# Kernel tuning notes

Hardware: AMD Instinct MI355X
Metric: run time of the kernel (lower is better)

The kernel has to match this reference:

```python
import jax, jax.numpy as jnp
import numpy as np

N_NODES = 50000
N_EDGES = 800000
IN_DIM, HID, OUT_DIM = 128, 64, 64


def setup_inputs() -> dict:
    key = jax.random.key(0)
    ks = jax.random.split(key, 12)
    inp = {
        "x": jax.random.normal(ks[0], (N_NODES, IN_DIM), dtype=jnp.float32),
        "edge_index": jax.random.randint(ks[1], (2, N_EDGES), 0, N_NODES, dtype=jnp.int32),
    }
    dims = [(IN_DIM, HID), (HID, HID), (HID, HID), (HID, HID), (HID, OUT_DIM)]
    for i, (di, do) in enumerate(dims, start=1):
        scale = (2.0 / (di + do)) ** 0.5  # glorot-like
        inp[f"W{i}"] = jax.random.normal(ks[1 + i], (di, do), dtype=jnp.float32) * scale
        inp[f"b{i}"] = jnp.zeros((do,), dtype=jnp.float32)
    return inp


def _edge_norm(edge_index, n_nodes):
    # GCNConv(improved=True): add self-loops with weight 2.0, symmetric norm.
    src, dst = edge_index[0], edge_index[1]
    loop = jnp.arange(n_nodes, dtype=edge_index.dtype)
    src_f = jnp.concatenate([src, loop])
    dst_f = jnp.concatenate([dst, loop])
    w = jnp.concatenate([
        jnp.ones((src.shape[0],), jnp.float32),
        jnp.full((n_nodes,), 2.0, jnp.float32),
    ])
    deg = jax.ops.segment_sum(w, dst_f, num_segments=n_nodes)
    dinv = jnp.where(deg > 0, jax.lax.rsqrt(deg), 0.0)
    norm = dinv[src_f] * w * dinv[dst_f]  # [E+N]
    return src_f, dst_f, norm


def reference(x, edge_index, W1, b1, W2, b2, W3, b3, W4, b4, W5, b5):
    n = x.shape[0]
    src_f, dst_f, norm = _edge_norm(edge_index, n)

    def conv(h, W, b):
        h = h @ W                                  # [N, d_out]
        msg = h[src_f] * norm[:, None]             # gather + edge normalize
        return jax.ops.segment_sum(msg, dst_f, num_segments=n) + b

    h = jax.nn.relu(conv(x, W1, b1))
    h = jax.nn.relu(conv(h, W2, b2))
    h = jax.nn.relu(conv(h, W3, b3))
    h = jax.nn.relu(conv(h, W4, b4))
    return conv(h, W5, b5)
```

## Files before the change

### kernel.cpp

```cpp
#include <hip/hip_runtime.h>
#include <hip/hip_fp16.h>

#define NN 50000
#define NE 800000

__device__ __forceinline__ float bf2f(unsigned short u) {
    union { unsigned int i; float f; } v; v.i = ((unsigned int)u) << 16; return v.f;
}
__device__ __forceinline__ unsigned short f2bf(float f) {
    union { float f; unsigned int i; } v; v.f = f;
    unsigned int r = v.i + 0x7fffu + ((v.i >> 16) & 1u);
    return (unsigned short)(r >> 16);
}
__device__ __forceinline__ float rdlane_f(float x, int l) {
    return __uint_as_float(__builtin_amdgcn_readlane(__float_as_uint(x), l));
}

__global__ void k_zero(float4* __restrict__ p, int n16) {
    int i = blockIdx.x * 256 + threadIdx.x;
    if (i < n16) p[i] = make_float4(0.f, 0.f, 0.f, 0.f);
}


__global__ void k_count(const int* __restrict__ dst, int* __restrict__ cnt, int E) {
    int e = blockIdx.x * 256 + threadIdx.x;
    if (e < E) atomicAdd(&cnt[dst[e]], 1);
}

__global__ void k_scanA(const int* __restrict__ cnt, int* __restrict__ row_ptr,
                        int* __restrict__ bsum, float* __restrict__ dinv, int N) {
    __shared__ int buf[256];
    int i = blockIdx.x * 256 + threadIdx.x;
    int v = (i < N) ? cnt[i] : 0;
    if (i < N) dinv[i] = rsqrtf(2.0f + (float)v);
    buf[threadIdx.x] = v;
    __syncthreads();
    for (int off = 1; off < 256; off <<= 1) {
        int t = (threadIdx.x >= off) ? buf[threadIdx.x - off] : 0;
        __syncthreads();
        buf[threadIdx.x] += t;
        __syncthreads();
    }
    if (i < N) row_ptr[i] = buf[threadIdx.x] - v;
    if (threadIdx.x == 255) bsum[blockIdx.x] = buf[255];
}

__global__ void k_scanB(int* __restrict__ bsum, int nb) {
    __shared__ int buf[256];
    int v = (threadIdx.x < nb) ? bsum[threadIdx.x] : 0;
    buf[threadIdx.x] = v;
    __syncthreads();
    for (int off = 1; off < 256; off <<= 1) {
        int t = (threadIdx.x >= off) ? buf[threadIdx.x - off] : 0;
        __syncthreads();
        buf[threadIdx.x] += t;
        __syncthreads();
    }
    if (threadIdx.x < nb) bsum[threadIdx.x] = buf[threadIdx.x] - v;
}

__global__ void k_scanC(int* __restrict__ row_ptr, const int* __restrict__ bsum,
                        int N, int E) {
    int i = blockIdx.x * 256 + threadIdx.x;
    if (i < N) row_ptr[i] += bsum[blockIdx.x];
    if (i == 0) row_ptr[N] = E;
}

__global__ void k_fill(const int* __restrict__ src, const int* __restrict__ dst,
                       const float* __restrict__ dinv, const int* __restrict__ row_ptr,
                       int* __restrict__ cursor, unsigned* __restrict__ csr, int E) {
    int e = blockIdx.x * 256 + threadIdx.x;
    if (e >= E) return;
    int s = src[e], d = dst[e];
    int pos = row_ptr[d] + atomicAdd(&cursor[d], 1);
    float nm = dinv[s] * dinv[d];
    csr[pos] = (unsigned)s | ((unsigned)__half_as_ushort(__float2half(nm)) << 16);
}


__global__ __launch_bounds__(256, 4) void k_gemm128(const float* __restrict__ X,
                                                    const float* __restrict__ W,
                                                    unsigned short* __restrict__ H, int N) {
    const int K = 128;
    __shared__ float Ws[K * 64];
    for (int i = threadIdx.x; i < K * 16; i += 256)
        ((float4*)Ws)[i] = ((const float4*)W)[i];
    __syncthreads();

    const int g  = threadIdx.x >> 3;
    const int c0 = (threadIdx.x & 7) * 8;
    const int r0 = blockIdx.x * 64 + g * 2;
    const int r1 = r0 + 1;
    const bool v0 = r0 < N, v1 = r1 < N;

    float a00=0,a01=0,a02=0,a03=0,a04=0,a05=0,a06=0,a07=0;
    float a10=0,a11=0,a12=0,a13=0,a14=0,a15=0,a16=0,a17=0;

    const float* x0 = X + (size_t)r0 * K;
    const float* x1 = X + (size_t)r1 * K;

#pragma unroll 1
    for (int k0 = 0; k0 < K; k0 += 4) {
        float4 xa = v0 ? *(const float4*)(x0 + k0) : make_float4(0, 0, 0, 0);
        float4 xb = v1 ? *(const float4*)(x1 + k0) : make_float4(0, 0, 0, 0);
#pragma unroll
        for (int kk = 0; kk < 4; ++kk) {
            const float xs0 = (kk == 0) ? xa.x : (kk == 1) ? xa.y : (kk == 2) ? xa.z : xa.w;
            const float xs1 = (kk == 0) ? xb.x : (kk == 1) ? xb.y : (kk == 2) ? xb.z : xb.w;
            const float* wr = &Ws[(k0 + kk) * 64 + c0];
            const float4 w0 = *(const float4*)(wr);
            const float4 w1 = *(const float4*)(wr + 4);
            a00 = fmaf(xs0, w0.x, a00); a01 = fmaf(xs0, w0.y, a01);
            a02 = fmaf(xs0, w0.z, a02); a03 = fmaf(xs0, w0.w, a03);
            a04 = fmaf(xs0, w1.x, a04); a05 = fmaf(xs0, w1.y, a05);
            a06 = fmaf(xs0, w1.z, a06); a07 = fmaf(xs0, w1.w, a07);
            a10 = fmaf(xs1, w0.x, a10); a11 = fmaf(xs1, w0.y, a11);
            a12 = fmaf(xs1, w0.z, a12); a13 = fmaf(xs1, w0.w, a13);
            a14 = fmaf(xs1, w1.x, a14); a15 = fmaf(xs1, w1.y, a15);
            a16 = fmaf(xs1, w1.z, a16); a17 = fmaf(xs1, w1.w, a17);
        }
    }

    if (v0) {
        uint4 p;
        p.x = (unsigned)f2bf(a00) | ((unsigned)f2bf(a01) << 16);
        p.y = (unsigned)f2bf(a02) | ((unsigned)f2bf(a03) << 16);
        p.z = (unsigned)f2bf(a04) | ((unsigned)f2bf(a05) << 16);
        p.w = (unsigned)f2bf(a06) | ((unsigned)f2bf(a07) << 16);
        *(uint4*)&H[(size_t)r0 * 64 + c0] = p;
    }
    if (v1) {
        uint4 p;
        p.x = (unsigned)f2bf(a10) | ((unsigned)f2bf(a11) << 16);
        p.y = (unsigned)f2bf(a12) | ((unsigned)f2bf(a13) << 16);
        p.z = (unsigned)f2bf(a14) | ((unsigned)f2bf(a15) << 16);
        p.w = (unsigned)f2bf(a16) | ((unsigned)f2bf(a17) << 16);
        *(uint4*)&H[(size_t)r1 * 64 + c0] = p;
    }
}


__device__ __forceinline__ void unpack(unsigned w, int& ss, float& nn) {
    ss = (int)(w & 0xffffu);
    nn = __half2float(__ushort_as_half((unsigned short)(w >> 16)));
}

template <bool RELU>
__device__ __forceinline__ void agg_row2(const unsigned short* __restrict__ H,
                                         const unsigned* __restrict__ csr,
                                         const float4& b4, float di0, float di1,
                                         int i0, int i1, int s0, int e0, int s1, int e1,
                                         int lane, int g, int c4,
                                         float4& r0, float4& r1) {
    ushort4 hs0 = *(const ushort4*)&H[(size_t)i0 * 64 + c4];
    ushort4 hs1 = *(const ushort4*)&H[(size_t)i1 * 64 + c4];

    int ee0 = s0 + lane, ee1 = s1 + lane;
    unsigned pk0 = (ee0 < e0) ? csr[ee0] : 0u;
    unsigned pk1 = (ee1 < e1) ? csr[ee1] : 0u;

    int m0 = e0 - s0; if (m0 > 64) m0 = 64;
    int m1 = e1 - s1; if (m1 > 64) m1 = 64;
    int nt0 = (m0 + 3) >> 2, nt1 = (m1 + 3) >> 2;
    int ntm = nt0 > nt1 ? nt0 : nt1;

    float4 acc0 = make_float4(0.f, 0.f, 0.f, 0.f);
    float4 acc1 = make_float4(0.f, 0.f, 0.f, 0.f);

#pragma unroll 4
    for (int t = 0; t < ntm; ++t) {
        int sl = t * 4 + g;
        if (t < nt0) {
            unsigned w = __shfl(pk0, sl);
            int ss; float nn; unpack(w, ss, nn);
            ushort4 h = *(const ushort4*)&H[(size_t)ss * 64 + c4];
            acc0.x = fmaf(bf2f(h.x), nn, acc0.x);
            acc0.y = fmaf(bf2f(h.y), nn, acc0.y);
            acc0.z = fmaf(bf2f(h.z), nn, acc0.z);
            acc0.w = fmaf(bf2f(h.w), nn, acc0.w);
        }
        if (t < nt1) {
            unsigned w = __shfl(pk1, sl);
            int ss; float nn; unpack(w, ss, nn);
            ushort4 h = *(const ushort4*)&H[(size_t)ss * 64 + c4];
            acc1.x = fmaf(bf2f(h.x), nn, acc1.x);
            acc1.y = fmaf(bf2f(h.y), nn, acc1.y);
            acc1.z = fmaf(bf2f(h.z), nn, acc1.z);
            acc1.w = fmaf(bf2f(h.w), nn, acc1.w);
        }
    }

    for (int base = s0 + 64; base < e0; base += 64) {
        int e = base + lane;
        unsigned pk = (e < e0) ? csr[e] : 0u;
        int m = e0 - base; if (m > 64) m = 64;
        int nt = (m + 3) >> 2;
        for (int t = 0; t < nt; ++t) {
            unsigned w = __shfl(pk, t * 4 + g);
            int ss; float nn; unpack(w, ss, nn);
            ushort4 h = *(const ushort4*)&H[(size_t)ss * 64 + c4];
            acc0.x = fmaf(bf2f(h.x), nn, acc0.x);
            acc0.y = fmaf(bf2f(h.y), nn, acc0.y);
            acc0.z = fmaf(bf2f(h.z), nn, acc0.z);
            acc0.w = fmaf(bf2f(h.w), nn, acc0.w);
        }
    }
    for (int base = s1 + 64; base < e1; base += 64) {
        int e = base + lane;
        unsigned pk = (e < e1) ? csr[e] : 0u;
        int m = e1 - base; if (m > 64) m = 64;
        int nt = (m + 3) >> 2;
        for (int t = 0; t < nt; ++t) {
            unsigned w = __shfl(pk, t * 4 + g);
            int ss; float nn; unpack(w, ss, nn);
            ushort4 h = *(const ushort4*)&H[(size_t)ss * 64 + c4];
            acc1.x = fmaf(bf2f(h.x), nn, acc1.x);
            acc1.y = fmaf(bf2f(h.y), nn, acc1.y);
            acc1.z = fmaf(bf2f(h.z), nn, acc1.z);
            acc1.w = fmaf(bf2f(h.w), nn, acc1.w);
        }
    }

#pragma unroll
    for (int d = 16; d <= 32; d <<= 1) {
        acc0.x += __shfl_xor(acc0.x, d); acc0.y += __shfl_xor(acc0.y, d);
        acc0.z += __shfl_xor(acc0.z, d); acc0.w += __shfl_xor(acc0.w, d);
        acc1.x += __shfl_xor(acc1.x, d); acc1.y += __shfl_xor(acc1.y, d);
        acc1.z += __shfl_xor(acc1.z, d); acc1.w += __shfl_xor(acc1.w, d);
    }

    float sa = 2.0f * di0 * di0, sb = 2.0f * di1 * di1;
    r0.x = acc0.x + sa * bf2f(hs0.x) + b4.x;
    r0.y = acc0.y + sa * bf2f(hs0.y) + b4.y;
    r0.z = acc0.z + sa * bf2f(hs0.z) + b4.z;
    r0.w = acc0.w + sa * bf2f(hs0.w) + b4.w;
    r1.x = acc1.x + sb * bf2f(hs1.x) + b4.x;
    r1.y = acc1.y + sb * bf2f(hs1.y) + b4.y;
    r1.z = acc1.z + sb * bf2f(hs1.z) + b4.z;
    r1.w = acc1.w + sb * bf2f(hs1.w) + b4.w;
    if (RELU) {
        r0.x = fmaxf(r0.x, 0.f); r0.y = fmaxf(r0.y, 0.f);
        r0.z = fmaxf(r0.z, 0.f); r0.w = fmaxf(r0.w, 0.f);
        r1.x = fmaxf(r1.x, 0.f); r1.y = fmaxf(r1.y, 0.f);
        r1.z = fmaxf(r1.z, 0.f); r1.w = fmaxf(r1.w, 0.f);
    }
}

__global__ __launch_bounds__(256, 8) void k_fused(const unsigned short* __restrict__ H,
                                                  const int* __restrict__ row_ptr,
                                                  const unsigned* __restrict__ csr,
                                                  const float* __restrict__ dinv,
                                                  const float* __restrict__ bias,
                                                  const float* __restrict__ Wn,
                                                  unsigned short* __restrict__ Hout, int N) {
    const int wid  = threadIdx.x >> 6;
    const int lane = threadIdx.x & 63;
    const int i0   = (blockIdx.x * 4 + wid) * 2;
    const int i1   = i0 + 1;
    const int g    = lane >> 4;
    const int c4   = (lane & 15) * 4;

    int idx = i0 + lane;
    int   rp = (lane <= 2) ? row_ptr[idx] : 0;
    float dv = (lane <  2) ? dinv[idx]    : 0.f;

    const float4 b4 = *(const float4*)&bias[c4];
    int s0 = __shfl(rp, 0), sm = __shfl(rp, 1), e1 = __shfl(rp, 2);
    float di0 = __shfl(dv, 0), di1 = __shfl(dv, 1);

    float4 r0, r1;
    agg_row2<true>(H, csr, b4, di0, di1, i0, i1, s0, sm, sm, e1,
                   lane, g, c4, r0, r1);

    float y0 = 0.f, y1 = 0.f;
#pragma unroll
    for (int q = 0; q < 16; ++q) {
        float w0 = Wn[(4 * q + 0) * 64 + lane];
        float w1 = Wn[(4 * q + 1) * 64 + lane];
        float w2 = Wn[(4 * q + 2) * 64 + lane];
        float w3 = Wn[(4 * q + 3) * 64 + lane];
        y0 = fmaf(rdlane_f(r0.x, q), w0, y0);
        y0 = fmaf(rdlane_f(r0.y, q), w1, y0);
        y0 = fmaf(rdlane_f(r0.z, q), w2, y0);
        y0 = fmaf(rdlane_f(r0.w, q), w3, y0);
        y1 = fmaf(rdlane_f(r1.x, q), w0, y1);
        y1 = fmaf(rdlane_f(r1.y, q), w1, y1);
        y1 = fmaf(rdlane_f(r1.z, q), w2, y1);
        y1 = fmaf(rdlane_f(r1.w, q), w3, y1);
    }
    Hout[(size_t)i0 * 64 + lane] = f2bf(y0);
    Hout[(size_t)i1 * 64 + lane] = f2bf(y1);
}

__global__ __launch_bounds__(256, 8) void k_agg_last(const unsigned short* __restrict__ H,
                                                     const int* __restrict__ row_ptr,
                                                     const unsigned* __restrict__ csr,
                                                     const float* __restrict__ dinv,
                                                     const float* __restrict__ bias,
                                                     float* __restrict__ out, int N) {
    const int wid  = threadIdx.x >> 6;
    const int lane = threadIdx.x & 63;
    const int i0   = (blockIdx.x * 4 + wid) * 2;
    const int i1   = i0 + 1;
    const int g    = lane >> 4;
    const int c4   = (lane & 15) * 4;

    const float4 b4 = *(const float4*)&bias[c4];

    int idx = i0 + lane;
    int   rp = (lane <= 2) ? row_ptr[idx] : 0;
    float dv = (lane <  2) ? dinv[idx]    : 0.f;
    int s0 = __shfl(rp, 0), sm = __shfl(rp, 1), e1 = __shfl(rp, 2);
    float di0 = __shfl(dv, 0), di1 = __shfl(dv, 1);

    float4 r0, r1;
    agg_row2<false>(H, csr, b4, di0, di1, i0, i1, s0, sm, sm, e1,
                    lane, g, c4, r0, r1);
    if (g == 0) {
        *(float4*)&out[(size_t)i0 * 64 + c4] = r0;
        *(float4*)&out[(size_t)i1 * 64 + c4] = r1;
    }
}


extern "C" void kernel_launch(void* const* d_in, const int* in_sizes, int n_in,
                              void* d_out, int out_size, void* d_ws, size_t ws_size,
                              hipStream_t stream) {
    (void)in_sizes; (void)n_in; (void)out_size; (void)ws_size;

    const float* x  = (const float*)d_in[0];
    const int*   ei = (const int*)d_in[1];
    const float* Wl[5] = {(const float*)d_in[2], (const float*)d_in[4], (const float*)d_in[6],
                          (const float*)d_in[8], (const float*)d_in[10]};
    const float* bl[5] = {(const float*)d_in[3], (const float*)d_in[5], (const float*)d_in[7],
                          (const float*)d_in[9], (const float*)d_in[11]};
    float* out = (float*)d_out;

    const int* src = ei;
    const int* dst = ei + NE;

    char* ws = (char*)d_ws;
    size_t off = 0;
    auto alloc = [&](size_t bytes) -> void* {
        void* p = ws + off;
        off += (bytes + 255) & ~(size_t)255;
        return p;
    };
    int*      cnt     = (int*)alloc(NN * 4);
    int*      cursor  = (int*)alloc(NN * 4);
    size_t zero_bytes = (size_t)((char*)(cursor + NN) - (char*)cnt);
    int*      row_ptr = (int*)alloc((NN + 1) * 4);
    int*      bsum    = (int*)alloc(256 * 4);
    float*    dinv    = (float*)alloc(NN * 4);
    unsigned* csr     = (unsigned*)alloc((size_t)NE * 4);
    unsigned short* Hb  = (unsigned short*)alloc((size_t)NN * 64 * 2);
    unsigned short* Hb2 = (unsigned short*)alloc((size_t)NN * 64 * 2);

    int n16 = (int)((zero_bytes + 15) / 16);
    k_zero<<<(n16 + 255) / 256, 256, 0, stream>>>((float4*)cnt, n16);

    int ebl = (NE + 255) / 256;
    int nbl = (NN + 255) / 256;
    int gg  = (NN + 63) / 64;
    k_count<<<ebl, 256, 0, stream>>>(dst, cnt, NE);
    k_scanA<<<nbl, 256, 0, stream>>>(cnt, row_ptr, bsum, dinv, NN);
    k_scanB<<<1, 256, 0, stream>>>(bsum, nbl);
    k_scanC<<<nbl, 256, 0, stream>>>(row_ptr, bsum, NN, NE);
    k_fill<<<ebl, 256, 0, stream>>>(src, dst, dinv, row_ptr, cursor, csr, NE);
    k_gemm128<<<gg, 256, 0, stream>>>(x, Wl[0], Hb, NN);

    int ga = NN / 8;

    k_fused<<<ga, 256, 0, stream>>>(Hb,  row_ptr, csr, dinv, bl[0], Wl[1], Hb2, NN);
    k_fused<<<ga, 256, 0, stream>>>(Hb2, row_ptr, csr, dinv, bl[1], Wl[2], Hb,  NN);
    k_fused<<<ga, 256, 0, stream>>>(Hb,  row_ptr, csr, dinv, bl[2], Wl[3], Hb2, NN);
    k_fused<<<ga, 256, 0, stream>>>(Hb2, row_ptr, csr, dinv, bl[3], Wl[4], Hb,  NN);
    k_agg_last<<<ga, 256, 0, stream>>>(Hb, row_ptr, csr, dinv, bl[4], out, NN);
}
```

Measured before the change: 270.0 us.

## Split feature matrix into two column planes and aggregate each half separately

Stores the bf16 hidden features as two planes of 32 columns each, so each aggregation pass gathers a 3.2MB plane that fits better in cache. Each layer is split into two kernels: the first aggregates the low half into an fp32 scratch buffer, the second aggregates the high half and applies the dense transform to both halves. The CSR edge list is read with nontemporal loads. In exchange the kernel count doubles, the CSR is traversed twice per layer, and an extra fp32 intermediate is written and read back.

```diff
diff --git a/kernel.cpp b/kernel.cpp
--- a/kernel.cpp
+++ b/kernel.cpp
@@ -14,6 +14,10 @@
 }
 __device__ __forceinline__ float rdlane_f(float x, int l) {
     return __uint_as_float(__builtin_amdgcn_readlane(__float_as_uint(x), l));
+}
+__device__ __forceinline__ void unpack(unsigned w, int& ss, float& nn) {
+    ss = (int)(w & 0xffffu);
+    nn = __half2float(__ushort_as_half((unsigned short)(w >> 16)));
 }
 
 __global__ void k_zero(float4* __restrict__ p, int n16) {
@@ -121,13 +125,15 @@
         }
     }
 
+    unsigned short* Hp = H + (size_t)(c0 >> 5) * NN * 32;
+    const int co = c0 & 31;
     if (v0) {
         uint4 p;
         p.x = (unsigned)f2bf(a00) | ((unsigned)f2bf(a01) << 16);
         p.y = (unsigned)f2bf(a02) | ((unsigned)f2bf(a03) << 16);
         p.z = (unsigned)f2bf(a04) | ((unsigned)f2bf(a05) << 16);
         p.w = (unsigned)f2bf(a06) | ((unsigned)f2bf(a07) << 16);
-        *(uint4*)&H[(size_t)r0 * 64 + c0] = p;
+        *(uint4*)&Hp[(size_t)r0 * 32 + co] = p;
     }
     if (v1) {
         uint4 p;
@@ -135,33 +141,29 @@
         p.y = (unsigned)f2bf(a12) | ((unsigned)f2bf(a13) << 16);
         p.z = (unsigned)f2bf(a14) | ((unsigned)f2bf(a15) << 16);
         p.w = (unsigned)f2bf(a16) | ((unsigned)f2bf(a17) << 16);
-        *(uint4*)&H[(size_t)r1 * 64 + c0] = p;
-    }
-}
-
-
-__device__ __forceinline__ void unpack(unsigned w, int& ss, float& nn) {
-    ss = (int)(w & 0xffffu);
-    nn = __half2float(__ushort_as_half((unsigned short)(w >> 16)));
-}
+        *(uint4*)&Hp[(size_t)r1 * 32 + co] = p;
+    }
+}
+
 
 template <bool RELU>
-__device__ __forceinline__ void agg_row2(const unsigned short* __restrict__ H,
-                                         const unsigned* __restrict__ csr,
-                                         const float4& b4, float di0, float di1,
-                                         int i0, int i1, int s0, int e0, int s1, int e1,
-                                         int lane, int g, int c4,
-                                         float4& r0, float4& r1) {
-    ushort4 hs0 = *(const ushort4*)&H[(size_t)i0 * 64 + c4];
-    ushort4 hs1 = *(const ushort4*)&H[(size_t)i1 * 64 + c4];
+__device__ __forceinline__ void agg_half2(const unsigned short* __restrict__ Hp,
+                                          const unsigned* __restrict__ csr,
+                                          const float* __restrict__ bias_h,
+                                          float di0, float di1,
+                                          int i0, int i1, int s0, int e0, int s1, int e1,
+                                          int lane, int g, int c4,
+                                          float4& r0, float4& r1) {
+    ushort4 hs0 = *(const ushort4*)&Hp[(size_t)i0 * 32 + c4];
+    ushort4 hs1 = *(const ushort4*)&Hp[(size_t)i1 * 32 + c4];
 
     int ee0 = s0 + lane, ee1 = s1 + lane;
-    unsigned pk0 = (ee0 < e0) ? csr[ee0] : 0u;
-    unsigned pk1 = (ee1 < e1) ? csr[ee1] : 0u;
+    unsigned pk0 = (ee0 < e0) ? __builtin_nontemporal_load(csr + ee0) : 0u;
+    unsigned pk1 = (ee1 < e1) ? __builtin_nontemporal_load(csr + ee1) : 0u;
 
     int m0 = e0 - s0; if (m0 > 64) m0 = 64;
     int m1 = e1 - s1; if (m1 > 64) m1 = 64;
-    int nt0 = (m0 + 3) >> 2, nt1 = (m1 + 3) >> 2;
+    int nt0 = (m0 + 7) >> 3, nt1 = (m1 + 7) >> 3;
     int ntm = nt0 > nt1 ? nt0 : nt1;
 
     float4 acc0 = make_float4(0.f, 0.f, 0.f, 0.f);
@@ -169,11 +171,11 @@
 
 #pragma unroll 4
     for (int t = 0; t < ntm; ++t) {
-        int sl = t * 4 + g;
+        int sl = t * 8 + g;
         if (t < nt0) {
             unsigned w = __shfl(pk0, sl);
             int ss; float nn; unpack(w, ss, nn);
-            ushort4 h = *(const ushort4*)&H[(size_t)ss * 64 + c4];
+            ushort4 h = *(const ushort4*)&Hp[(size_t)ss * 32 + c4];
             acc0.x = fmaf(bf2f(h.x), nn, acc0.x);
             acc0.y = fmaf(bf2f(h.y), nn, acc0.y);
             acc0.z = fmaf(bf2f(h.z), nn, acc0.z);
@@ -182,7 +184,7 @@
         if (t < nt1) {
             unsigned w = __shfl(pk1, sl);
             int ss; float nn; unpack(w, ss, nn);
-            ushort4 h = *(const ushort4*)&H[(size_t)ss * 64 + c4];
+            ushort4 h = *(const ushort4*)&Hp[(size_t)ss * 32 + c4];
             acc1.x = fmaf(bf2f(h.x), nn, acc1.x);
             acc1.y = fmaf(bf2f(h.y), nn, acc1.y);
             acc1.z = fmaf(bf2f(h.z), nn, acc1.z);
@@ -192,13 +194,13 @@
 
     for (int base = s0 + 64; base < e0; base += 64) {
         int e = base + lane;
-        unsigned pk = (e < e0) ? csr[e] : 0u;
+        unsigned pk = (e < e0) ? __builtin_nontemporal_load(csr + e) : 0u;
         int m = e0 - base; if (m > 64) m = 64;
-        int nt = (m + 3) >> 2;
+        int nt = (m + 7) >> 3;
         for (int t = 0; t < nt; ++t) {
-            unsigned w = __shfl(pk, t * 4 + g);
+            unsigned w = __shfl(pk, t * 8 + g);
             int ss; float nn; unpack(w, ss, nn);
-            ushort4 h = *(const ushort4*)&H[(size_t)ss * 64 + c4];
+            ushort4 h = *(const ushort4*)&Hp[(size_t)ss * 32 + c4];
             acc0.x = fmaf(bf2f(h.x), nn, acc0.x);
             acc0.y = fmaf(bf2f(h.y), nn, acc0.y);
             acc0.z = fmaf(bf2f(h.z), nn, acc0.z);
@@ -207,13 +209,13 @@
     }
     for (int base = s1 + 64; base < e1; base += 64) {
         int e = base + lane;
-        unsigned pk = (e < e1) ? csr[e] : 0u;
+        unsigned pk = (e < e1) ? __builtin_nontemporal_load(csr + e) : 0u;
         int m = e1 - base; if (m > 64) m = 64;
-        int nt = (m + 3) >> 2;
+        int nt = (m + 7) >> 3;
         for (int t = 0; t < nt; ++t) {
-            unsigned w = __shfl(pk, t * 4 + g);
+            unsigned w = __shfl(pk, t * 8 + g);
             int ss; float nn; unpack(w, ss, nn);
-            ushort4 h = *(const ushort4*)&H[(size_t)ss * 64 + c4];
+            ushort4 h = *(const ushort4*)&Hp[(size_t)ss * 32 + c4];
             acc1.x = fmaf(bf2f(h.x), nn, acc1.x);
             acc1.y = fmaf(bf2f(h.y), nn, acc1.y);
             acc1.z = fmaf(bf2f(h.z), nn, acc1.z);
@@ -222,13 +224,14 @@
     }
 
 #pragma unroll
-    for (int d = 16; d <= 32; d <<= 1) {
+    for (int d = 8; d <= 32; d <<= 1) {
         acc0.x += __shfl_xor(acc0.x, d); acc0.y += __shfl_xor(acc0.y, d);
         acc0.z += __shfl_xor(acc0.z, d); acc0.w += __shfl_xor(acc0.w, d);
         acc1.x += __shfl_xor(acc1.x, d); acc1.y += __shfl_xor(acc1.y, d);
         acc1.z += __shfl_xor(acc1.z, d); acc1.w += __shfl_xor(acc1.w, d);
     }
 
+    float4 b4 = *(const float4*)&bias_h[c4];
     float sa = 2.0f * di0 * di0, sb = 2.0f * di1 * di1;
     r0.x = acc0.x + sa * bf2f(hs0.x) + b4.x;
     r0.y = acc0.y + sa * bf2f(hs0.y) + b4.y;
@@ -246,80 +249,117 @@
     }
 }
 
-__global__ __launch_bounds__(256, 8) void k_fused(const unsigned short* __restrict__ H,
-                                                  const int* __restrict__ row_ptr,
-                                                  const unsigned* __restrict__ csr,
-                                                  const float* __restrict__ dinv,
-                                                  const float* __restrict__ bias,
-                                                  const float* __restrict__ Wn,
-                                                  unsigned short* __restrict__ Hout, int N) {
+__device__ __forceinline__ void load_meta(const int* __restrict__ row_ptr,
+                                          const float* __restrict__ dinv,
+                                          int i0, int lane,
+                                          int& s0, int& sm, int& e1,
+                                          float& di0, float& di1) {
+    int idx = i0 + lane;
+    int   rp = (lane <= 2) ? row_ptr[idx] : 0;
+    float dv = (lane <  2) ? dinv[idx]    : 0.f;
+    s0 = __shfl(rp, 0); sm = __shfl(rp, 1); e1 = __shfl(rp, 2);
+    di0 = __shfl(dv, 0); di1 = __shfl(dv, 1);
+}
+
+__global__ __launch_bounds__(256, 8) void k_aggA(const unsigned short* __restrict__ Hpl,
+                                                 const int* __restrict__ row_ptr,
+                                                 const unsigned* __restrict__ csr,
+                                                 const float* __restrict__ dinv,
+                                                 const float* __restrict__ bias,
+                                                 float* __restrict__ A0, int N) {
     const int wid  = threadIdx.x >> 6;
     const int lane = threadIdx.x & 63;
     const int i0   = (blockIdx.x * 4 + wid) * 2;
     const int i1   = i0 + 1;
-    const int g    = lane >> 4;
-    const int c4   = (lane & 15) * 4;
-
-    int idx = i0 + lane;
-    int   rp = (lane <= 2) ? row_ptr[idx] : 0;
-    float dv = (lane <  2) ? dinv[idx]    : 0.f;
-
-    const float4 b4 = *(const float4*)&bias[c4];
-    int s0 = __shfl(rp, 0), sm = __shfl(rp, 1), e1 = __shfl(rp, 2);
-    float di0 = __shfl(dv, 0), di1 = __shfl(dv, 1);
+    const int g    = lane >> 3;
+    const int c4   = (lane & 7) * 4;
+
+    int s0, sm, e1; float di0, di1;
+    load_meta(row_ptr, dinv, i0, lane, s0, sm, e1, di0, di1);
 
     float4 r0, r1;
-    agg_row2<true>(H, csr, b4, di0, di1, i0, i1, s0, sm, sm, e1,
-                   lane, g, c4, r0, r1);
-
-    float y0 = 0.f, y1 = 0.f;
-#pragma unroll
-    for (int q = 0; q < 16; ++q) {
-        float w0 = Wn[(4 * q + 0) * 64 + lane];
-        float w1 = Wn[(4 * q + 1) * 64 + lane];
-        float w2 = Wn[(4 * q + 2) * 64 + lane];
-        float w3 = Wn[(4 * q + 3) * 64 + lane];
-        y0 = fmaf(rdlane_f(r0.x, q), w0, y0);
-        y0 = fmaf(rdlane_f(r0.y, q), w1, y0);
-        y0 = fmaf(rdlane_f(r0.z, q), w2, y0);
-        y0 = fmaf(rdlane_f(r0.w, q), w3, y0);
-        y1 = fmaf(rdlane_f(r1.x, q), w0, y1);
-        y1 = fmaf(rdlane_f(r1.y, q), w1, y1);
-        y1 = fmaf(rdlane_f(r1.z, q), w2, y1);
-        y1 = fmaf(rdlane_f(r1.w, q), w3, y1);
-    }
-    Hout[(size_t)i0 * 64 + lane] = f2bf(y0);
-    Hout[(size_t)i1 * 64 + lane] = f2bf(y1);
-}
-
-__global__ __launch_bounds__(256, 8) void k_agg_last(const unsigned short* __restrict__ H,
-                                                     const int* __restrict__ row_ptr,
-                                                     const unsigned* __restrict__ csr,
-                                                     const float* __restrict__ dinv,
-                                                     const float* __restrict__ bias,
-                                                     float* __restrict__ out, int N) {
+    agg_half2<true>(Hpl, csr, bias, di0, di1, i0, i1, s0, sm, sm, e1,
+                    lane, g, c4, r0, r1);
+
+    if (g == 0) *(float4*)&A0[(size_t)i0 * 32 + c4] = r0;
+    if (g == 1) *(float4*)&A0[(size_t)i1 * 32 + c4] = r1;
+}
+
+__global__ __launch_bounds__(256, 8) void k_aggB(const unsigned short* __restrict__ Hpl1,
+                                                 const int* __restrict__ row_ptr,
+                                                 const unsigned* __restrict__ csr,
+                                                 const float* __restrict__ dinv,
+                                                 const float* __restrict__ bias,
+                                                 const float* __restrict__ A0,
+                                                 const float* __restrict__ Wn,
+                                                 unsigned short* __restrict__ Hout, int N) {
     const int wid  = threadIdx.x >> 6;
     const int lane = threadIdx.x & 63;
     const int i0   = (blockIdx.x * 4 + wid) * 2;
     const int i1   = i0 + 1;
-    const int g    = lane >> 4;
-    const int c4   = (lane & 15) * 4;
-
-    const float4 b4 = *(const float4*)&bias[c4];
-
-    int idx = i0 + lane;
-    int   rp = (lane <= 2) ? row_ptr[idx] : 0;
-    float dv = (lane <  2) ? dinv[idx]    : 0.f;
-    int s0 = __shfl(rp, 0), sm = __shfl(rp, 1), e1 = __shfl(rp, 2);
-    float di0 = __shfl(dv, 0), di1 = __shfl(dv, 1);
+    const int g    = lane >> 3;
+    const int c4   = (lane & 7) * 4;
+
+    int s0, sm, e1; float di0, di1;
+    load_meta(row_ptr, dinv, i0, lane, s0, sm, e1, di0, di1);
+
+    float a0v = (lane < 32) ? A0[(size_t)i0 * 32 + lane]
+                            : A0[(size_t)i1 * 32 + (lane - 32)];
 
     float4 r0, r1;
-    agg_row2<false>(H, csr, b4, di0, di1, i0, i1, s0, sm, sm, e1,
+    agg_half2<true>(Hpl1, csr, bias + 32, di0, di1, i0, i1, s0, sm, sm, e1,
                     lane, g, c4, r0, r1);
-    if (g == 0) {
-        *(float4*)&out[(size_t)i0 * 64 + c4] = r0;
-        *(float4*)&out[(size_t)i1 * 64 + c4] = r1;
-    }
+
+    float y0 = 0.f, y1 = 0.f;
+#pragma unroll
+    for (int q = 0; q < 32; ++q) {
+        float w = Wn[q * 64 + lane];
+        y0 = fmaf(rdlane_f(a0v, q),      w, y0);
+        y1 = fmaf(rdlane_f(a0v, 32 + q), w, y1);
+    }
+#pragma unroll
+    for (int p = 0; p < 8; ++p) {
+        float w0 = Wn[(32 + 4 * p + 0) * 64 + lane];
+        float w1 = Wn[(32 + 4 * p + 1) * 64 + lane];
+        float w2 = Wn[(32 + 4 * p + 2) * 64 + lane];
+        float w3 = Wn[(32 + 4 * p + 3) * 64 + lane];
+        y0 = fmaf(rdlane_f(r0.x, p), w0, y0);
+        y0 = fmaf(rdlane_f(r0.y, p), w1, y0);
+        y0 = fmaf(rdlane_f(r0.z, p), w2, y0);
+        y0 = fmaf(rdlane_f(r0.w, p), w3, y0);
+        y1 = fmaf(rdlane_f(r1.x, p), w0, y1);
+        y1 = fmaf(rdlane_f(r1.y, p), w1, y1);
+        y1 = fmaf(rdlane_f(r1.z, p), w2, y1);
+        y1 = fmaf(rdlane_f(r1.w, p), w3, y1);
+    }
+    unsigned short* Hp = Hout + (size_t)(lane >> 5) * NN * 32;
+    Hp[(size_t)i0 * 32 + (lane & 31)] = f2bf(y0);
+    Hp[(size_t)i1 * 32 + (lane & 31)] = f2bf(y1);
+}
+
+template <int HALF>
+__global__ __launch_bounds__(256, 8) void k_last(const unsigned short* __restrict__ Hpl,
+                                                 const int* __restrict__ row_ptr,
+                                                 const unsigned* __restrict__ csr,
+                                                 const float* __restrict__ dinv,
+                                                 const float* __restrict__ bias,
+                                                 float* __restrict__ out, int N) {
+    const int wid  = threadIdx.x >> 6;
+    const int lane = threadIdx.x & 63;
+    const int i0   = (blockIdx.x * 4 + wid) * 2;
+    const int i1   = i0 + 1;
+    const int g    = lane >> 3;
+    const int c4   = (lane & 7) * 4;
+
+    int s0, sm, e1; float di0, di1;
+    load_meta(row_ptr, dinv, i0, lane, s0, sm, e1, di0, di1);
+
+    float4 r0, r1;
+    agg_half2<false>(Hpl, csr, bias + HALF * 32, di0, di1, i0, i1, s0, sm, sm, e1,
+                     lane, g, c4, r0, r1);
+
+    if (g == 0) *(float4*)&out[(size_t)i0 * 64 + HALF * 32 + c4] = r0;
+    if (g == 1) *(float4*)&out[(size_t)i1 * 64 + HALF * 32 + c4] = r1;
 }
 
 
@@ -355,6 +395,7 @@
     unsigned* csr     = (unsigned*)alloc((size_t)NE * 4);
     unsigned short* Hb  = (unsigned short*)alloc((size_t)NN * 64 * 2);
     unsigned short* Hb2 = (unsigned short*)alloc((size_t)NN * 64 * 2);
+    float*    A0      = (float*)alloc((size_t)NN * 32 * 4);
 
     int n16 = (int)((zero_bytes + 15) / 16);
     k_zero<<<(n16 + 255) / 256, 256, 0, stream>>>((float4*)cnt, n16);
@@ -369,11 +410,17 @@
     k_fill<<<ebl, 256, 0, stream>>>(src, dst, dinv, row_ptr, cursor, csr, NE);
     k_gemm128<<<gg, 256, 0, stream>>>(x, Wl[0], Hb, NN);
 
+    const size_t PL = (size_t)NN * 32;
     int ga = NN / 8;
 
-    k_fused<<<ga, 256, 0, stream>>>(Hb,  row_ptr, csr, dinv, bl[0], Wl[1], Hb2, NN);
-    k_fused<<<ga, 256, 0, stream>>>(Hb2, row_ptr, csr, dinv, bl[1], Wl[2], Hb,  NN);
-    k_fused<<<ga, 256, 0, stream>>>(Hb,  row_ptr, csr, dinv, bl[2], Wl[3], Hb2, NN);
-    k_fused<<<ga, 256, 0, stream>>>(Hb2, row_ptr, csr, dinv, bl[3], Wl[4], Hb,  NN);
-    k_agg_last<<<ga, 256, 0, stream>>>(Hb, row_ptr, csr, dinv, bl[4], out, NN);
-}
+    unsigned short* Hc = Hb;
+    unsigned short* Hn = Hb2;
+    for (int l = 0; l < 4; ++l) {
+        k_aggA<<<ga, 256, 0, stream>>>(Hc,      row_ptr, csr, dinv, bl[l], A0, NN);
+        k_aggB<<<ga, 256, 0, stream>>>(Hc + PL, row_ptr, csr, dinv, bl[l], A0,
+                                       Wl[l + 1], Hn, NN);
+        unsigned short* t = Hc; Hc = Hn; Hn = t;
+    }
+    k_last<0><<<ga, 256, 0, stream>>>(Hc,      row_ptr, csr, dinv, bl[4], out, NN);
+    k_last<1><<<ga, 256, 0, stream>>>(Hc + PL, row_ptr, csr, dinv, bl[4], out, NN);
+}
```

New measurement: 340.4 us. 26.1% more time.
